# Kernel tuning notes

Measured on AMD Instinct MI355X. Metric: run time of the kernel, lower is better.

The kernel has to match this reference:

```python
import jax, jax.numpy as jnp
import numpy as np

N = 50000      # nodes
E = 600000     # edges
G = 512        # graphs in batch
F_IN = 128     # input node features
H = 128        # hidden size (both layers)
PH = 128       # pool/classifier hidden size


def setup_inputs() -> dict:
    key = jax.random.key(0)
    ks = jax.random.split(key, 12)
    def lin(k, fi, fo):
        return (jax.random.normal(k, (fi, fo), jnp.float32) / np.sqrt(fi)).astype(jnp.float32)
    return {
        "x": jax.random.normal(ks[0], (N, F_IN), jnp.float32),
        "edge_index": jax.random.randint(ks[1], (2, E), 0, N),
        "batch": jnp.sort(jax.random.randint(ks[2], (N,), 0, G)),
        "W1": lin(ks[3], F_IN, H), "b1": jnp.zeros((H,), jnp.float32),
        "ln1_g": jnp.ones((H,), jnp.float32), "ln1_b": jnp.zeros((H,), jnp.float32),
        "W2": lin(ks[4], H, H), "b2": jnp.zeros((H,), jnp.float32),
        "ln2_g": jnp.ones((H,), jnp.float32), "ln2_b": jnp.zeros((H,), jnp.float32),
        "gate_w1": lin(ks[5], H, PH), "gate_b1": jnp.zeros((PH,), jnp.float32),
        "gate_w2": lin(ks[6], PH, 1), "gate_b2": jnp.zeros((1,), jnp.float32),
        "cls_w1": lin(ks[7], H, PH), "cls_b1": jnp.zeros((PH,), jnp.float32),
        "cls_w2": lin(ks[8], PH, 2), "cls_b2": jnp.zeros((2,), jnp.float32),
    }


def _layer_norm(h, g, b):
    m = h.mean(-1, keepdims=True)
    v = ((h - m) ** 2).mean(-1, keepdims=True)
    return (h - m) * jax.lax.rsqrt(v + 1e-5) * g + b


def _gcn(x, src, dst, norm, W, b):
    # GCNConv: x' = D^{-1/2} (A+I) D^{-1/2} (x W) + b
    h = x @ W
    out = jax.ops.segment_sum(h[src] * norm[:, None], dst, num_segments=N)
    return out + b


def reference(x, edge_index, batch, W1, b1, ln1_g, ln1_b, W2, b2, ln2_g, ln2_b,
              gate_w1, gate_b1, gate_w2, gate_b2, cls_w1, cls_b1, cls_w2, cls_b2):
    loops = jnp.arange(N, dtype=edge_index.dtype)
    src = jnp.concatenate([edge_index[0], loops])
    dst = jnp.concatenate([edge_index[1], loops])
    deg = jax.ops.segment_sum(jnp.ones_like(src, dtype=x.dtype), dst, num_segments=N)
    dinv = jnp.where(deg > 0, jax.lax.rsqrt(jnp.maximum(deg, 1e-12)), 0.0)
    norm = dinv[src] * dinv[dst]  # [(E+N)]

    h = jax.nn.relu(_layer_norm(_gcn(x, src, dst, norm, W1, b1), ln1_g, ln1_b))
    h = jax.nn.relu(_layer_norm(_gcn(h, src, dst, norm, W2, b2), ln2_g, ln2_b))

    # GlobalAttention pooling: gate MLP -> scatter softmax over graphs -> weighted sum
    gate = (jax.nn.relu(h @ gate_w1 + gate_b1) @ gate_w2 + gate_b2)[:, 0]  # [N]
    gmax = jax.ops.segment_max(gate, batch, num_segments=G)
    a = jnp.exp(gate - gmax[batch])
    denom = jax.ops.segment_sum(a, batch, num_segments=G)
    alpha = a / denom[batch]
    pooled = jax.ops.segment_sum(alpha[:, None] * h, batch, num_segments=G)  # [G, H]

    logits = jax.nn.relu(pooled @ cls_w1 + cls_b1) @ cls_w2 + cls_b2  # [G, 2]
    return logits
```

## Files before the change

### kernel.cpp

```cpp
#include <hip/hip_runtime.h>
#include <hip/hip_bf16.h>

typedef short s8v __attribute__((ext_vector_type(8)));
typedef float f4v __attribute__((ext_vector_type(4)));

#define LDA 136

__device__ __forceinline__ unsigned short f2bf(float f) {
  unsigned int u = __builtin_bit_cast(unsigned int, f);
  unsigned int r = u + 0x7fffu + ((u >> 16) & 1u);
  return (unsigned short)(r >> 16);
}
__device__ __forceinline__ float bf2f(unsigned short s) {
  return __builtin_bit_cast(float, ((unsigned int)s) << 16);
}
__device__ __forceinline__ float bflo(unsigned int v) {
  return __builtin_bit_cast(float, (unsigned int)(v << 16));
}
__device__ __forceinline__ float bfhi(unsigned int v) {
  return __builtin_bit_cast(float, (unsigned int)(v & 0xffff0000u));
}
__device__ __forceinline__ unsigned int packbf(float a, float b) {
  return (unsigned int)f2bf(a) | ((unsigned int)f2bf(b) << 16);
}

__device__ __forceinline__ int lower_bound_i(const int* a, int n, int key) {
  int lo = 0, hi = n;
  while (lo < hi) { int mid = (lo + hi) >> 1; if (a[mid] < key) lo = mid + 1; else hi = mid; }
  return lo;
}

__device__ __forceinline__ float gather_node(
    int i, int sub, const int* __restrict__ offs, const int* __restrict__ col,
    const float* __restrict__ dinv, const uint4* __restrict__ hu, float acc[8]) {
  float di = dinv[i];
  uint4 hv = hu[(size_t)i * 16 + sub];
  acc[0] = bflo(hv.x) * di; acc[1] = bfhi(hv.x) * di;
  acc[2] = bflo(hv.y) * di; acc[3] = bfhi(hv.y) * di;
  acc[4] = bflo(hv.z) * di; acc[5] = bfhi(hv.z) * di;
  acc[6] = bflo(hv.w) * di; acc[7] = bfhi(hv.w) * di;
  int b0 = offs[i], b1 = offs[i + 1];
  int e = b0;
  for (; e + 4 <= b1; e += 4) {
    int s0 = col[e], s1 = col[e + 1], s2 = col[e + 2], s3 = col[e + 3];
    uint4 h0 = hu[(size_t)s0 * 16 + sub];
    uint4 h1 = hu[(size_t)s1 * 16 + sub];
    uint4 h2 = hu[(size_t)s2 * 16 + sub];
    uint4 h3 = hu[(size_t)s3 * 16 + sub];
    float n0 = dinv[s0], n1 = dinv[s1], n2 = dinv[s2], n3 = dinv[s3];
    acc[0] += bflo(h0.x) * n0 + bflo(h1.x) * n1 + bflo(h2.x) * n2 + bflo(h3.x) * n3;
    acc[1] += bfhi(h0.x) * n0 + bfhi(h1.x) * n1 + bfhi(h2.x) * n2 + bfhi(h3.x) * n3;
    acc[2] += bflo(h0.y) * n0 + bflo(h1.y) * n1 + bflo(h2.y) * n2 + bflo(h3.y) * n3;
    acc[3] += bfhi(h0.y) * n0 + bfhi(h1.y) * n1 + bfhi(h2.y) * n2 + bfhi(h3.y) * n3;
    acc[4] += bflo(h0.z) * n0 + bflo(h1.z) * n1 + bflo(h2.z) * n2 + bflo(h3.z) * n3;
    acc[5] += bfhi(h0.z) * n0 + bfhi(h1.z) * n1 + bfhi(h2.z) * n2 + bfhi(h3.z) * n3;
    acc[6] += bflo(h0.w) * n0 + bflo(h1.w) * n1 + bflo(h2.w) * n2 + bflo(h3.w) * n3;
    acc[7] += bfhi(h0.w) * n0 + bfhi(h1.w) * n1 + bfhi(h2.w) * n2 + bfhi(h3.w) * n3;
  }
  for (; e < b1; ++e) {
    int s0 = col[e];
    uint4 h0 = hu[(size_t)s0 * 16 + sub];
    float n0 = dinv[s0];
    acc[0] += bflo(h0.x) * n0; acc[1] += bfhi(h0.x) * n0;
    acc[2] += bflo(h0.y) * n0; acc[3] += bfhi(h0.y) * n0;
    acc[4] += bflo(h0.z) * n0; acc[5] += bfhi(h0.z) * n0;
    acc[6] += bflo(h0.w) * n0; acc[7] += bfhi(h0.w) * n0;
  }
  return di;
}

__device__ __forceinline__ uint4 ln_relu_pack(
    float v[8], int sub, const float* __restrict__ gam, const float* __restrict__ bet) {
  float s = 0.f, q = 0.f;
#pragma unroll
  for (int j = 0; j < 8; ++j) { s += v[j]; q += v[j] * v[j]; }
#pragma unroll
  for (int o = 1; o < 16; o <<= 1) {
    s += __shfl_xor(s, o);
    q += __shfl_xor(q, o);
  }
  float m = s * (1.0f / 128.0f);
  float var = q * (1.0f / 128.0f) - m * m;
  float rs = rsqrtf(var + 1e-5f);
  float4 g0 = reinterpret_cast<const float4*>(gam)[sub * 2];
  float4 g1 = reinterpret_cast<const float4*>(gam)[sub * 2 + 1];
  float4 e0 = reinterpret_cast<const float4*>(bet)[sub * 2];
  float4 e1 = reinterpret_cast<const float4*>(bet)[sub * 2 + 1];
  uint4 ov;
  ov.x = packbf(fmaxf((v[0] - m) * rs * g0.x + e0.x, 0.f), fmaxf((v[1] - m) * rs * g0.y + e0.y, 0.f));
  ov.y = packbf(fmaxf((v[2] - m) * rs * g0.z + e0.z, 0.f), fmaxf((v[3] - m) * rs * g0.w + e0.w, 0.f));
  ov.z = packbf(fmaxf((v[4] - m) * rs * g1.x + e1.x, 0.f), fmaxf((v[5] - m) * rs * g1.y + e1.y, 0.f));
  ov.w = packbf(fmaxf((v[6] - m) * rs * g1.z + e1.z, 0.f), fmaxf((v[7] - m) * rs * g1.w + e1.w, 0.f));
  return ov;
}

__device__ __forceinline__ void scale_bias(
    float acc[8], float di, int sub, const float* __restrict__ bias, float v[8]) {
  float4 b0v = reinterpret_cast<const float4*>(bias)[sub * 2];
  float4 b1v = reinterpret_cast<const float4*>(bias)[sub * 2 + 1];
  v[0] = acc[0] * di + b0v.x; v[1] = acc[1] * di + b0v.y;
  v[2] = acc[2] * di + b0v.z; v[3] = acc[3] * di + b0v.w;
  v[4] = acc[4] * di + b1v.x; v[5] = acc[5] * di + b1v.y;
  v[6] = acc[6] * di + b1v.z; v[7] = acc[7] * di + b1v.w;
}

__global__ __launch_bounds__(256) void packhist(
    const float* __restrict__ Wa, const float* __restrict__ Wb, const float* __restrict__ Wc,
    unsigned short* __restrict__ P, const int* __restrict__ dst,
    unsigned int* __restrict__ Hist, int E) {
  __shared__ unsigned int cnt[256];
  int bid = blockIdx.x;
  int t = threadIdx.x;
  if (bid >= 384) {
    int hb = bid - 384;
    cnt[t] = 0u;
    __syncthreads();
    int chunk = (E + 63) >> 6;
    int lo = hb * chunk, hi = min(E, lo + chunk);
    for (int e = lo + t; e < hi; e += 256)
      atomicAdd(&cnt[((unsigned int)dst[e]) >> 8], 1u);
    __syncthreads();
    Hist[hb * 256 + t] = cnt[t];
    return;
  }
  int gidx = bid * 256 + t;
  int which = gidx >> 15;
  int idx = gidx & 32767;
  const float* W = (which == 0) ? Wa : (which == 1) ? Wb : Wc;
  int j = idx & 15;
  int lane = (idx >> 4) & 63;
  int tt = (idx >> 10) & 7;
  int c = (idx >> 13) & 3;
  int k = c * 32 + (lane >> 4) * 8 + (j & 7);
  int nn = tt * 16 + (lane & 15);
  float f = W[k * 128 + nn];
  unsigned short hi16 = f2bf(f);
  unsigned short outv = (j < 8) ? hi16 : f2bf(f - bf2f(hi16));
  P[gidx] = outv;
}

__global__ __launch_bounds__(256) void scanbase(
    unsigned int* __restrict__ Hist, unsigned int* __restrict__ Base,
    unsigned int* __restrict__ Bstart, int* __restrict__ offs, int n, int E) {
  __shared__ int sh[256];
  int t = threadIdx.x;
  unsigned int run = 0;
  for (int b = 0; b < 64; ++b) {
    Base[b * 256 + t] = run;
    run += Hist[b * 256 + t];
  }
  int v = (int)run;
  sh[t] = v;
  __syncthreads();
  for (int o = 1; o < 256; o <<= 1) {
    int add = (t >= o) ? sh[t - o] : 0;
    __syncthreads();
    sh[t] += add;
    __syncthreads();
  }
  unsigned int pre = (unsigned int)(sh[t] - v);
  Bstart[t] = pre;
  for (int b = 0; b < 64; ++b) Base[b * 256 + t] += pre;
  if (t == 0) offs[n] = E;
}

__global__ __launch_bounds__(256) void gemm1_scatter(
    const float* __restrict__ in, const unsigned short* __restrict__ P,
    unsigned short* __restrict__ out, int n,
    const int* __restrict__ src, const int* __restrict__ dst,
    const unsigned int* __restrict__ Base, unsigned int* __restrict__ EP,
    int E, int gemmBlocks) {
  __shared__ unsigned int cur[256];
  int tid = threadIdx.x;
  if ((int)blockIdx.x >= gemmBlocks) {
    int sb = (int)blockIdx.x - gemmBlocks;
    cur[tid] = Base[sb * 256 + tid];
    __syncthreads();
    int chunk = (E + 63) >> 6;
    int lo = sb * chunk, hi = min(E, lo + chunk);
    for (int e = lo + tid; e < hi; e += 256) {
      unsigned int d = (unsigned int)dst[e];
      unsigned int s = (unsigned int)src[e];
      unsigned int pos = atomicAdd(&cur[d >> 8], 1u);
      EP[pos] = ((d & 255u) << 16) | s;
    }
    return;
  }
  int wave = tid >> 6, lane = tid & 63;
  int quad = lane >> 4, c16 = lane & 15;
  int base = blockIdx.x * 64 + wave * 16;
  int m = base + c16;

  f4v acc[8];
#pragma unroll
  for (int t = 0; t < 8; ++t) acc[t] = (f4v){0.f, 0.f, 0.f, 0.f};

  for (int c = 0; c < 4; ++c) {
    s8v ah, al;
    float v[8];
    if (m < n) {
      const float4* xp = reinterpret_cast<const float4*>(in + (size_t)m * 128 + c * 32 + quad * 8);
      float4 v0 = xp[0], v1 = xp[1];
      v[0] = v0.x; v[1] = v0.y; v[2] = v0.z; v[3] = v0.w;
      v[4] = v1.x; v[5] = v1.y; v[6] = v1.z; v[7] = v1.w;
    } else {
#pragma unroll
      for (int j = 0; j < 8; ++j) v[j] = 0.f;
    }
#pragma unroll
    for (int j = 0; j < 8; ++j) {
      unsigned short h = f2bf(v[j]);
      ah[j] = (short)h;
      al[j] = (short)f2bf(v[j] - bf2f(h));
    }
#pragma unroll
    for (int t = 0; t < 8; ++t) {
      const s8v* bp = reinterpret_cast<const s8v*>(&P[((c * 8 + t) * 64 + lane) * 16]);
      s8v bh = bp[0], bl = bp[1];
      acc[t] = __builtin_amdgcn_mfma_f32_16x16x32_bf16(ah, bh, acc[t], 0, 0, 0);
      acc[t] = __builtin_amdgcn_mfma_f32_16x16x32_bf16(ah, bl, acc[t], 0, 0, 0);
      acc[t] = __builtin_amdgcn_mfma_f32_16x16x32_bf16(al, bh, acc[t], 0, 0, 0);
    }
  }
#pragma unroll
  for (int t = 0; t < 8; ++t)
#pragma unroll
    for (int r = 0; r < 4; ++r) {
      int mm = base + quad * 4 + r;
      if (mm < n) out[(size_t)mm * 128 + t * 16 + c16] = f2bf(acc[t][r]);
    }
}

__global__ __launch_bounds__(256) void fine_csr(
    const unsigned int* __restrict__ EP, const unsigned int* __restrict__ Bstart,
    int* __restrict__ offs, float* __restrict__ dinv, int* __restrict__ col, int n) {
  __shared__ unsigned int cnt[256];
  __shared__ int sh[256];
  __shared__ unsigned int cur[256];
  int bk = blockIdx.x;
  int t = threadIdx.x;
  unsigned int rlo = Bstart[bk];
  unsigned int rhi = (bk < 255) ? Bstart[bk + 1] : rlo;
  cnt[t] = 0u;
  __syncthreads();
  for (unsigned int i = rlo + t; i < rhi; i += 256)
    atomicAdd(&cnt[EP[i] >> 16], 1u);
  __syncthreads();
  int v = (int)cnt[t];
  sh[t] = v;
  __syncthreads();
  for (int o = 1; o < 256; o <<= 1) {
    int add = (t >= o) ? sh[t - o] : 0;
    __syncthreads();
    sh[t] += add;
    __syncthreads();
  }
  int pre = sh[t] - v;
  int node = bk * 256 + t;
  if (node < n) {
    offs[node] = (int)(rlo + pre);
    dinv[node] = rsqrtf((float)(v + 1));
  }
  cur[t] = rlo + (unsigned int)pre;
  __syncthreads();
  for (unsigned int i = rlo + t; i < rhi; i += 256) {
    unsigned int w = EP[i];
    unsigned int dl = w >> 16;
    unsigned int pos = atomicAdd(&cur[dl], 1u);
    col[pos] = (int)(w & 0xffffu);
  }
}

__global__ __launch_bounds__(256) void gather_gemm(
    const int* __restrict__ offs, const int* __restrict__ col,
    const float* __restrict__ dinv, const unsigned short* __restrict__ h,
    const float* __restrict__ bias, const float* __restrict__ gam,
    const float* __restrict__ bet, const unsigned short* __restrict__ P,
    unsigned short* __restrict__ out, int n) {
  __shared__ unsigned short A[32 * LDA];
  int tid = threadIdx.x;
  int wave = tid >> 6, lane = tid & 63;
  int grp = lane >> 4, sub = lane & 15;
  const uint4* hu = reinterpret_cast<const uint4*>(h);
  int blk = blockIdx.x * 32;
  for (int it = 0; it < 2; ++it) {
    int li = it * 16 + wave * 4 + grp;
    int i = blk + li;
    uint4 ov;
    if (i < n) {
      float acc[8], v[8];
      float di = gather_node(i, sub, offs, col, dinv, hu, acc);
      scale_bias(acc, di, sub, bias, v);
      ov = ln_relu_pack(v, sub, gam, bet);
    } else {
      ov = make_uint4(0u, 0u, 0u, 0u);
    }
    *reinterpret_cast<uint4*>(&A[li * LDA + sub * 8]) = ov;
  }
  __syncthreads();
  int quad = lane >> 4, c16 = lane & 15;
  int rowgrp = wave & 1, colhalf = wave >> 1;
  f4v acc[4];
#pragma unroll
  for (int t = 0; t < 4; ++t) acc[t] = (f4v){0.f, 0.f, 0.f, 0.f};
  int liA = rowgrp * 16 + c16;
  for (int c = 0; c < 4; ++c) {
    s8v ah = *reinterpret_cast<const s8v*>(&A[liA * LDA + c * 32 + quad * 8]);
#pragma unroll
    for (int t4 = 0; t4 < 4; ++t4) {
      int t = colhalf * 4 + t4;
      const s8v* bp = reinterpret_cast<const s8v*>(&P[((c * 8 + t) * 64 + lane) * 16]);
      s8v bh = bp[0], bl = bp[1];
      acc[t4] = __builtin_amdgcn_mfma_f32_16x16x32_bf16(ah, bh, acc[t4], 0, 0, 0);
      acc[t4] = __builtin_amdgcn_mfma_f32_16x16x32_bf16(ah, bl, acc[t4], 0, 0, 0);
    }
  }
#pragma unroll
  for (int t4 = 0; t4 < 4; ++t4) {
    int t = colhalf * 4 + t4;
#pragma unroll
    for (int r = 0; r < 4; ++r) {
      int mm = blk + rowgrp * 16 + quad * 4 + r;
      if (mm < n) out[(size_t)mm * 128 + t * 16 + c16] = f2bf(acc[t4][r]);
    }
  }
}

__global__ __launch_bounds__(256) void gather_gate(
    const int* __restrict__ offs, const int* __restrict__ col,
    const float* __restrict__ dinv, const unsigned short* __restrict__ h,
    const float* __restrict__ bias, const float* __restrict__ gam,
    const float* __restrict__ bet, const unsigned short* __restrict__ P,
    const float* __restrict__ gb1, const float* __restrict__ gw2,
    const float* __restrict__ gb2, unsigned short* __restrict__ hout,
    float* __restrict__ gate, int n) {
  __shared__ unsigned short A[32 * LDA];
  __shared__ float pbuf[4][16];
  int tid = threadIdx.x;
  int wave = tid >> 6, lane = tid & 63;
  int grp = lane >> 4, sub = lane & 15;
  const uint4* hu = reinterpret_cast<const uint4*>(h);
  int blk = blockIdx.x * 32;
  for (int it = 0; it < 2; ++it) {
    int li = it * 16 + wave * 4 + grp;
    int i = blk + li;
    uint4 ov;
    if (i < n) {
      float acc[8], v[8];
      float di = gather_node(i, sub, offs, col, dinv, hu, acc);
      scale_bias(acc, di, sub, bias, v);
      ov = ln_relu_pack(v, sub, gam, bet);
      reinterpret_cast<uint4*>(hout)[(size_t)i * 16 + sub] = ov;
    } else {
      ov = make_uint4(0u, 0u, 0u, 0u);
    }
    *reinterpret_cast<uint4*>(&A[li * LDA + sub * 8]) = ov;
  }
  __syncthreads();
  int quad = lane >> 4, c16 = lane & 15;
  int rowgrp = wave & 1, colhalf = wave >> 1;
  f4v acc[4];
#pragma unroll
  for (int t = 0; t < 4; ++t) acc[t] = (f4v){0.f, 0.f, 0.f, 0.f};
  int liA = rowgrp * 16 + c16;
  for (int c = 0; c < 4; ++c) {
    s8v ah = *reinterpret_cast<const s8v*>(&A[liA * LDA + c * 32 + quad * 8]);
#pragma unroll
    for (int t4 = 0; t4 < 4; ++t4) {
      int t = colhalf * 4 + t4;
      const s8v* bp = reinterpret_cast<const s8v*>(&P[((c * 8 + t) * 64 + lane) * 16]);
      s8v bh = bp[0], bl = bp[1];
      acc[t4] = __builtin_amdgcn_mfma_f32_16x16x32_bf16(ah, bh, acc[t4], 0, 0, 0);
      acc[t4] = __builtin_amdgcn_mfma_f32_16x16x32_bf16(ah, bl, acc[t4], 0, 0, 0);
    }
  }
  float bv[4], g2[4];
#pragma unroll
  for (int t4 = 0; t4 < 4; ++t4) {
    int t = colhalf * 4 + t4;
    bv[t4] = gb1[t * 16 + c16];
    g2[t4] = gw2[t * 16 + c16];
  }
#pragma unroll
  for (int r = 0; r < 4; ++r) {
    float p = 0.f;
#pragma unroll
    for (int t4 = 0; t4 < 4; ++t4)
      p += fmaxf(acc[t4][r] + bv[t4], 0.f) * g2[t4];
#pragma unroll
    for (int o = 1; o < 16; o <<= 1) p += __shfl_xor(p, o);
    if (c16 == 0) pbuf[wave][quad * 4 + r] = p;
  }
  __syncthreads();
  if (tid < 32) {
    int rg = tid >> 4, local = tid & 15;
    int mm = blk + tid;
    if (mm < n) gate[mm] = pbuf[rg][local] + pbuf[rg + 2][local] + gb2[0];
  }
}

__global__ __launch_bounds__(256) void pool_cls(
    float* __restrict__ gate, const unsigned short* __restrict__ h,
    const int* __restrict__ batch,
    const float* __restrict__ w1, const float* __restrict__ b1,
    const float* __restrict__ w2, const float* __restrict__ b2,
    float* __restrict__ out, int n) {
  int g = blockIdx.x;
  int tid = threadIdx.x;
  __shared__ float red[256];
  __shared__ float red2[256];
  __shared__ float p[128];
  __shared__ float r[128];
  int lo = lower_bound_i(batch, n, g);
  int hi = lower_bound_i(batch, n, g + 1);
  if (lo >= hi) {
    if (tid < 128) p[tid] = 0.0f;
  } else {
    float m = -3.0e38f;
    for (int i = lo + tid; i < hi; i += 256) m = fmaxf(m, gate[i]);
    red[tid] = m;
    __syncthreads();
#pragma unroll
    for (int o = 128; o > 0; o >>= 1) {
      if (tid < o) red[tid] = fmaxf(red[tid], red[tid + o]);
      __syncthreads();
    }
    m = red[0];
    __syncthreads();
    float s = 0.0f;
    for (int i = lo + tid; i < hi; i += 256) {
      float e = __expf(gate[i] - m);
      gate[i] = e;
      s += e;
    }
    red[tid] = s;
    __syncthreads();
#pragma unroll
    for (int o = 128; o > 0; o >>= 1) {
      if (tid < o) red[tid] += red[tid + o];
      __syncthreads();
    }
    float inv = 1.0f / red[0];
    __syncthreads();
    const unsigned int* hu = reinterpret_cast<const unsigned int*>(h);
    int j = tid & 63, rgp = tid >> 6;
    float a0 = 0.f, a1 = 0.f;
    int i = lo + rgp;
    for (; i + 12 < hi; i += 16) {
      unsigned int p0 = hu[(size_t)i * 64 + j];
      unsigned int p1 = hu[(size_t)(i + 4) * 64 + j];
      unsigned int p2 = hu[(size_t)(i + 8) * 64 + j];
      unsigned int p3 = hu[(size_t)(i + 12) * 64 + j];
      float w0 = gate[i], w1v = gate[i + 4], w2v = gate[i + 8], w3v = gate[i + 12];
      a0 += bflo(p0) * w0 + bflo(p1) * w1v + bflo(p2) * w2v + bflo(p3) * w3v;
      a1 += bfhi(p0) * w0 + bfhi(p1) * w1v + bfhi(p2) * w2v + bfhi(p3) * w3v;
    }
    for (; i < hi; i += 4) {
      unsigned int p0 = hu[(size_t)i * 64 + j];
      float w0 = gate[i];
      a0 += bflo(p0) * w0;
      a1 += bfhi(p0) * w0;
    }
    red[tid] = a0;
    red2[tid] = a1;
    __syncthreads();
    if (tid < 64) {
      p[2 * tid]     = (red[tid] + red[tid + 64] + red[tid + 128] + red[tid + 192]) * inv;
      p[2 * tid + 1] = (red2[tid] + red2[tid + 64] + red2[tid + 128] + red2[tid + 192]) * inv;
    }
  }
  __syncthreads();
  int j = tid & 127, half = tid >> 7;
  float acc = 0.0f;
#pragma unroll 8
  for (int k = half * 64; k < half * 64 + 64; ++k)
    acc = fmaf(p[k], w1[k * 128 + j], acc);
  red[tid] = acc;
  __syncthreads();
  if (tid < 128) r[tid] = fmaxf(red[tid] + red[tid + 128] + b1[tid], 0.0f);
  __syncthreads();
  if (tid < 2) {
    float a = 0.0f;
    for (int k = 0; k < 128; ++k) a = fmaf(r[k], w2[k * 2 + tid], a);
    out[g * 2 + tid] = a + b2[tid];
  }
}

static inline size_t alup(size_t x) { return (x + 255) & ~(size_t)255; }

extern "C" void kernel_launch(void* const* d_in, const int* in_sizes, int n_in,
                              void* d_out, int out_size, void* d_ws, size_t ws_size,
                              hipStream_t stream) {
  const float* x    = (const float*)d_in[0];
  const int*   ei   = (const int*)d_in[1];
  const int*   bat  = (const int*)d_in[2];
  const float* W1   = (const float*)d_in[3];
  const float* b1   = (const float*)d_in[4];
  const float* ln1g = (const float*)d_in[5];
  const float* ln1b = (const float*)d_in[6];
  const float* W2   = (const float*)d_in[7];
  const float* b2   = (const float*)d_in[8];
  const float* ln2g = (const float*)d_in[9];
  const float* ln2b = (const float*)d_in[10];
  const float* gw1  = (const float*)d_in[11];
  const float* gb1  = (const float*)d_in[12];
  const float* gw2  = (const float*)d_in[13];
  const float* gb2  = (const float*)d_in[14];
  const float* cw1  = (const float*)d_in[15];
  const float* cb1  = (const float*)d_in[16];
  const float* cw2  = (const float*)d_in[17];
  const float* cb2  = (const float*)d_in[18];

  const int N = in_sizes[2];
  const int E = in_sizes[1] / 2;
  const int G = out_size / 2;
  const int* src = ei;
  const int* dst = ei + E;

  int mfmaB = (N + 63) / 64;
  int fuseB = (N + 31) / 32;
  int NB = (N + 255) / 256;

  char* base = (char*)d_ws;
  unsigned int* Hist = (unsigned int*)base;   base += alup((size_t)64 * 256 * 4);
  unsigned int* Base = (unsigned int*)base;   base += alup((size_t)64 * 256 * 4);
  unsigned int* Bstart = (unsigned int*)base; base += alup((size_t)256 * 4);
  unsigned int* EP = (unsigned int*)base;     base += alup((size_t)E * 4);
  float* dinv = (float*)base;                 base += alup((size_t)N * 4);
  int* offs = (int*)base;                     base += alup((size_t)(N + 1) * 4);
  int* col = (int*)base;                      base += alup((size_t)E * 4);
  unsigned short* pW = (unsigned short*)base; base += alup((size_t)3 * 32768 * 2);
  unsigned short* hbuf = (unsigned short*)base;  base += alup((size_t)N * 128 * 2);
  unsigned short* hbuf2 = (unsigned short*)base; base += alup((size_t)N * 128 * 2);
  unsigned short* hout = (unsigned short*)base;  base += alup((size_t)N * 128 * 2);
  float* gate = (float*)base;                 base += alup((size_t)N * 4);

  unsigned short* pW1 = pW;
  unsigned short* pW2 = pW + 32768;
  unsigned short* pG1 = pW + 65536;

  float* out = (float*)d_out;

  packhist<<<384 + 64, 256, 0, stream>>>(W1, W2, gw1, pW, dst, Hist, E);
  scanbase<<<1, 256, 0, stream>>>(Hist, Base, Bstart, offs, N, E);
  gemm1_scatter<<<mfmaB + 64, 256, 0, stream>>>(x, pW1, hbuf, N,
                                                src, dst, Base, EP, E, mfmaB);
  fine_csr<<<NB, 256, 0, stream>>>(EP, Bstart, offs, dinv, col, N);
  gather_gemm<<<fuseB, 256, 0, stream>>>(offs, col, dinv, hbuf, b1, ln1g, ln1b,
                                         pW2, hbuf2, N);
  gather_gate<<<fuseB, 256, 0, stream>>>(offs, col, dinv, hbuf2, b2, ln2g, ln2b,
                                         pG1, gb1, gw2, gb2, hout, gate, N);
  pool_cls<<<G, 256, 0, stream>>>(gate, hout, bat, cw1, cb1, cw2, cb2, out, N);
}
```

Measured before the change: 247.2 us.

## Fold scan kernel into scatter and CSR kernels; prescale layer-2 features by dinv

Removes the single-block scanbase kernel. Each scatter block and each fine_csr block now recomputes the bucket prefix sums from the histogram in shared memory, which saves a launch and a serial one-block step at the cost of redundant scan work per block. It also multiplies the gather_gemm output rows by dinv of the source node, so the layer-2 gather in gather_gate can sum neighbor rows without a per-edge dinv load and multiply. Layer 1 still uses the weighted gather.

```diff
diff --git a/kernel.cpp b/kernel.cpp
--- a/kernel.cpp
+++ b/kernel.cpp
@@ -69,6 +69,41 @@
   return di;
 }
 
+__device__ __forceinline__ void gather_sum(
+    int i, int sub, const int* __restrict__ offs, const int* __restrict__ col,
+    const uint4* __restrict__ hu, float acc[8]) {
+  uint4 hv = hu[(size_t)i * 16 + sub];
+  acc[0] = bflo(hv.x); acc[1] = bfhi(hv.x);
+  acc[2] = bflo(hv.y); acc[3] = bfhi(hv.y);
+  acc[4] = bflo(hv.z); acc[5] = bfhi(hv.z);
+  acc[6] = bflo(hv.w); acc[7] = bfhi(hv.w);
+  int b0 = offs[i], b1 = offs[i + 1];
+  int e = b0;
+  for (; e + 4 <= b1; e += 4) {
+    int s0 = col[e], s1 = col[e + 1], s2 = col[e + 2], s3 = col[e + 3];
+    uint4 h0 = hu[(size_t)s0 * 16 + sub];
+    uint4 h1 = hu[(size_t)s1 * 16 + sub];
+    uint4 h2 = hu[(size_t)s2 * 16 + sub];
+    uint4 h3 = hu[(size_t)s3 * 16 + sub];
+    acc[0] += bflo(h0.x) + bflo(h1.x) + bflo(h2.x) + bflo(h3.x);
+    acc[1] += bfhi(h0.x) + bfhi(h1.x) + bfhi(h2.x) + bfhi(h3.x);
+    acc[2] += bflo(h0.y) + bflo(h1.y) + bflo(h2.y) + bflo(h3.y);
+    acc[3] += bfhi(h0.y) + bfhi(h1.y) + bfhi(h2.y) + bfhi(h3.y);
+    acc[4] += bflo(h0.z) + bflo(h1.z) + bflo(h2.z) + bflo(h3.z);
+    acc[5] += bfhi(h0.z) + bfhi(h1.z) + bfhi(h2.z) + bfhi(h3.z);
+    acc[6] += bflo(h0.w) + bflo(h1.w) + bflo(h2.w) + bflo(h3.w);
+    acc[7] += bfhi(h0.w) + bfhi(h1.w) + bfhi(h2.w) + bfhi(h3.w);
+  }
+  for (; e < b1; ++e) {
+    int s0 = col[e];
+    uint4 h0 = hu[(size_t)s0 * 16 + sub];
+    acc[0] += bflo(h0.x); acc[1] += bfhi(h0.x);
+    acc[2] += bflo(h0.y); acc[3] += bfhi(h0.y);
+    acc[4] += bflo(h0.z); acc[5] += bfhi(h0.z);
+    acc[6] += bflo(h0.w); acc[7] += bfhi(h0.w);
+  }
+}
+
 __device__ __forceinline__ uint4 ln_relu_pack(
     float v[8], int sub, const float* __restrict__ gam, const float* __restrict__ bet) {
   float s = 0.f, q = 0.f;
@@ -139,42 +174,33 @@
   P[gidx] = outv;
 }
 
-__global__ __launch_bounds__(256) void scanbase(
-    unsigned int* __restrict__ Hist, unsigned int* __restrict__ Base,
-    unsigned int* __restrict__ Bstart, int* __restrict__ offs, int n, int E) {
-  __shared__ int sh[256];
-  int t = threadIdx.x;
-  unsigned int run = 0;
-  for (int b = 0; b < 64; ++b) {
-    Base[b * 256 + t] = run;
-    run += Hist[b * 256 + t];
-  }
-  int v = (int)run;
-  sh[t] = v;
-  __syncthreads();
-  for (int o = 1; o < 256; o <<= 1) {
-    int add = (t >= o) ? sh[t - o] : 0;
-    __syncthreads();
-    sh[t] += add;
-    __syncthreads();
-  }
-  unsigned int pre = (unsigned int)(sh[t] - v);
-  Bstart[t] = pre;
-  for (int b = 0; b < 64; ++b) Base[b * 256 + t] += pre;
-  if (t == 0) offs[n] = E;
-}
-
 __global__ __launch_bounds__(256) void gemm1_scatter(
     const float* __restrict__ in, const unsigned short* __restrict__ P,
     unsigned short* __restrict__ out, int n,
     const int* __restrict__ src, const int* __restrict__ dst,
-    const unsigned int* __restrict__ Base, unsigned int* __restrict__ EP,
+    const unsigned int* __restrict__ Hist, unsigned int* __restrict__ EP,
     int E, int gemmBlocks) {
   __shared__ unsigned int cur[256];
+  __shared__ int scanb[256];
   int tid = threadIdx.x;
   if ((int)blockIdx.x >= gemmBlocks) {
     int sb = (int)blockIdx.x - gemmBlocks;
-    cur[tid] = Base[sb * 256 + tid];
+    unsigned int before = 0, total = 0;
+    for (int b = 0; b < 64; ++b) {
+      unsigned int hv = Hist[b * 256 + tid];
+      if (b < sb) before += hv;
+      total += hv;
+    }
+    int v = (int)total;
+    scanb[tid] = v;
+    __syncthreads();
+    for (int o = 1; o < 256; o <<= 1) {
+      int add = (tid >= o) ? scanb[tid - o] : 0;
+      __syncthreads();
+      scanb[tid] += add;
+      __syncthreads();
+    }
+    cur[tid] = (unsigned int)(scanb[tid] - v) + before;
     __syncthreads();
     int chunk = (E + 63) >> 6;
     int lo = sb * chunk, hi = min(E, lo + chunk);
@@ -232,15 +258,29 @@
 }
 
 __global__ __launch_bounds__(256) void fine_csr(
-    const unsigned int* __restrict__ EP, const unsigned int* __restrict__ Bstart,
-    int* __restrict__ offs, float* __restrict__ dinv, int* __restrict__ col, int n) {
+    const unsigned int* __restrict__ EP, const unsigned int* __restrict__ Hist,
+    int* __restrict__ offs, float* __restrict__ dinv, int* __restrict__ col, int n, int E) {
   __shared__ unsigned int cnt[256];
   __shared__ int sh[256];
   __shared__ unsigned int cur[256];
+  __shared__ int tot[256];
+  __shared__ int bst[256];
   int bk = blockIdx.x;
   int t = threadIdx.x;
-  unsigned int rlo = Bstart[bk];
-  unsigned int rhi = (bk < 255) ? Bstart[bk + 1] : rlo;
+  unsigned int total = 0;
+  for (int b = 0; b < 64; ++b) total += Hist[b * 256 + t];
+  tot[t] = (int)total;
+  bst[t] = (int)total;
+  __syncthreads();
+  for (int o = 1; o < 256; o <<= 1) {
+    int add = (t >= o) ? bst[t - o] : 0;
+    __syncthreads();
+    bst[t] += add;
+    __syncthreads();
+  }
+  unsigned int rlo = (unsigned int)(bst[bk] - tot[bk]);
+  unsigned int rhi = rlo + (unsigned int)tot[bk];
+  if (bk == 0 && t == 0) offs[n] = E;
   cnt[t] = 0u;
   __syncthreads();
   for (unsigned int i = rlo + t; i < rhi; i += 256)
@@ -315,13 +355,19 @@
       acc[t4] = __builtin_amdgcn_mfma_f32_16x16x32_bf16(ah, bl, acc[t4], 0, 0, 0);
     }
   }
+  float dv[4];
+#pragma unroll
+  for (int r = 0; r < 4; ++r) {
+    int mm = blk + rowgrp * 16 + quad * 4 + r;
+    dv[r] = (mm < n) ? dinv[mm] : 0.f;
+  }
 #pragma unroll
   for (int t4 = 0; t4 < 4; ++t4) {
     int t = colhalf * 4 + t4;
 #pragma unroll
     for (int r = 0; r < 4; ++r) {
       int mm = blk + rowgrp * 16 + quad * 4 + r;
-      if (mm < n) out[(size_t)mm * 128 + t * 16 + c16] = f2bf(acc[t4][r]);
+      if (mm < n) out[(size_t)mm * 128 + t * 16 + c16] = f2bf(acc[t4][r] * dv[r]);
     }
   }
 }
@@ -347,8 +393,8 @@
     uint4 ov;
     if (i < n) {
       float acc[8], v[8];
-      float di = gather_node(i, sub, offs, col, dinv, hu, acc);
-      scale_bias(acc, di, sub, bias, v);
+      gather_sum(i, sub, offs, col, hu, acc);
+      scale_bias(acc, dinv[i], sub, bias, v);
       ov = ln_relu_pack(v, sub, gam, bet);
       reinterpret_cast<uint4*>(hout)[(size_t)i * 16 + sub] = ov;
     } else {
@@ -523,8 +569,6 @@
 
   char* base = (char*)d_ws;
   unsigned int* Hist = (unsigned int*)base;   base += alup((size_t)64 * 256 * 4);
-  unsigned int* Base = (unsigned int*)base;   base += alup((size_t)64 * 256 * 4);
-  unsigned int* Bstart = (unsigned int*)base; base += alup((size_t)256 * 4);
   unsigned int* EP = (unsigned int*)base;     base += alup((size_t)E * 4);
   float* dinv = (float*)base;                 base += alup((size_t)N * 4);
   int* offs = (int*)base;                     base += alup((size_t)(N + 1) * 4);
@@ -542,10 +586,9 @@
   float* out = (float*)d_out;
 
   packhist<<<384 + 64, 256, 0, stream>>>(W1, W2, gw1, pW, dst, Hist, E);
-  scanbase<<<1, 256, 0, stream>>>(Hist, Base, Bstart, offs, N, E);
   gemm1_scatter<<<mfmaB + 64, 256, 0, stream>>>(x, pW1, hbuf, N,
-                                                src, dst, Base, EP, E, mfmaB);
-  fine_csr<<<NB, 256, 0, stream>>>(EP, Bstart, offs, dinv, col, N);
+                                                src, dst, Hist, EP, E, mfmaB);
+  fine_csr<<<NB, 256, 0, stream>>>(EP, Hist, offs, dinv, col, N, E);
   gather_gemm<<<fuseB, 256, 0, stream>>>(offs, col, dinv, hbuf, b1, ln1g, ln1b,
                                          pW2, hbuf2, N);
   gather_gate<<<fuseB, 256, 0, stream>>>(offs, col, dinv, hbuf2, b2, ln2g, ln2b,
```

After: 245.2 us. No clear change (-0.8%).
